# Performance work log

Hardware: AMD Instinct MI355X
Metric: run time of the kernel (lower is better)

## Reference

```python
import jax, jax.numpy as jnp
import numpy as np

N_HEADS = 16
HEAD_DIM = 64
LN_EPS = 1e-5


def setup_inputs() -> dict:
    key = jax.random.key(0)
    k1, k2, k3 = jax.random.split(key, 3)
    b, n, d = 4, 2048, 1024
    inner = N_HEADS * HEAD_DIM  # 1024
    x = jax.random.normal(k1, (b, n, d), dtype=jnp.float32)
    ln_gamma = jnp.ones((d,), dtype=jnp.float32)
    ln_beta = jnp.zeros((d,), dtype=jnp.float32)
    # torch Linear weights are [out_features, in_features]
    W_qkv = jax.random.normal(k2, (3 * inner, d), dtype=jnp.float32) * (d ** -0.5)
    W_out = jax.random.normal(k3, (d, inner), dtype=jnp.float32) * (inner ** -0.5)
    return {"x": x, "ln_gamma": ln_gamma, "ln_beta": ln_beta,
            "W_qkv": W_qkv, "W_out": W_out}


def reference(x, ln_gamma, ln_beta, W_qkv, W_out):
    b, n, d = x.shape
    scale = HEAD_DIM ** -0.5
    # LayerNorm over last dim
    mu = jnp.mean(x, axis=-1, keepdims=True)
    var = jnp.mean(jnp.square(x - mu), axis=-1, keepdims=True)
    xn = (x - mu) * jax.lax.rsqrt(var + LN_EPS) * ln_gamma + ln_beta
    # QKV projection (Linear, no bias): y = x @ W^T
    qkv = jnp.einsum('bnd,ed->bne', xn, W_qkv)  # [b, n, 3*inner]
    qkv = qkv.reshape(b, n, 3, N_HEADS, HEAD_DIM)
    q, k, v = (jnp.transpose(qkv[:, :, i], (0, 2, 1, 3)) for i in range(3))  # [b,h,n,hd]
    scores = jnp.einsum('bhqd,bhkd->bhqk', q, k) * scale  # [b,h,n,n]
    attn = jax.nn.softmax(scores, axis=-1)
    out = jnp.einsum('bhqk,bhkd->bhqd', attn, v)  # [b,h,n,hd]
    out = jnp.transpose(out, (0, 2, 1, 3)).reshape(b, n, N_HEADS * HEAD_DIM)
    return jnp.einsum('bni,di->bnd', out, W_out)
```

## Files before the change

kernel.cpp:

```cpp
#include <hip/hip_runtime.h>


typedef _Float16 h16;
typedef __attribute__((ext_vector_type(8))) _Float16 h16x8;
typedef __attribute__((ext_vector_type(4))) _Float16 h16x4;
typedef __attribute__((ext_vector_type(4))) float f32x4;

#define B_ 4
#define S_ 2048
#define D_ 1024

static __device__ __forceinline__ void async16(void* lds, const void* g) {
  __builtin_amdgcn_global_load_lds((const __attribute__((address_space(1))) void*)g,
                                   (__attribute__((address_space(3))) void*)lds,
                                   16, 0, 0);
}

static __device__ __forceinline__ float ex2(float x) {
  float r;
  asm("v_exp_f32 %0, %1" : "=v"(r) : "v"(x));
  return r;
}

__global__ __launch_bounds__(256) void ln_k(const float* __restrict__ x,
                                            const float* __restrict__ g,
                                            const float* __restrict__ be,
                                            h16* __restrict__ xn) {
  const int row = blockIdx.x;
  const int tid = threadIdx.x;
  const float4 v = ((const float4*)(x + (size_t)row * D_))[tid];
  float s = v.x + v.y + v.z + v.w;
  float s2 = v.x * v.x + v.y * v.y + v.z * v.z + v.w * v.w;
#pragma unroll
  for (int msk = 1; msk < 64; msk <<= 1) {
    s += __shfl_xor(s, msk);
    s2 += __shfl_xor(s2, msk);
  }
  __shared__ float red[8];
  const int wv = tid >> 6, ln = tid & 63;
  if (ln == 0) { red[wv] = s; red[wv + 4] = s2; }
  __syncthreads();
  s = red[0] + red[1] + red[2] + red[3];
  s2 = red[4] + red[5] + red[6] + red[7];
  const float mu = s * (1.f / D_);
  const float rs = rsqrtf(s2 * (1.f / D_) - mu * mu + 1e-5f);
  const float4 gv = ((const float4*)g)[tid];
  const float4 bv = ((const float4*)be)[tid];
  h16x4 o;
  o[0] = (h16)((v.x - mu) * rs * gv.x + bv.x);
  o[1] = (h16)((v.y - mu) * rs * gv.y + bv.y);
  o[2] = (h16)((v.z - mu) * rs * gv.z + bv.z);
  o[3] = (h16)((v.w - mu) * rs * gv.w + bv.w);
  *(h16x4*)(xn + (size_t)row * D_ + tid * 4) = o;
}

__global__ __launch_bounds__(256) void cvt_k(const float* __restrict__ in,
                                             h16* __restrict__ o, int n4) {
  const int i = blockIdx.x * 256 + threadIdx.x;
  if (i >= n4) return;
  const float4 v = ((const float4*)in)[i];
  h16x4 r;
  r[0] = (h16)v.x; r[1] = (h16)v.y; r[2] = (h16)v.z; r[3] = (h16)v.w;
  *(h16x4*)(o + (size_t)i * 4) = r;
}

__global__ __launch_bounds__(256) void vt_k(const h16* __restrict__ qkv,
                                            h16* __restrict__ vT) {
  __shared__ h16 T[64 * 72];
  const int tid = threadIdx.x;
  const int kv0 = blockIdx.x * 64;
  const int bh = blockIdx.y;
  const int b = bh >> 4, h = bh & 15;
#pragma unroll
  for (int it = 0; it < 2; ++it) {
    const int s = tid + it * 256;
    const int kv = s >> 3, sl = s & 7;
    const int wsl = sl ^ ((kv >> 3) & 7);
    const h16x8 v = *(const h16x8*)(qkv + (size_t)(b * S_ + kv0 + kv) * 3072 + 2048 + h * 64 + sl * 8);
    *(h16x8*)(T + kv * 72 + wsl * 8) = v;
  }
  __syncthreads();
#pragma unroll
  for (int it = 0; it < 2; ++it) {
    const int s = tid + it * 256;
    const int d = s >> 3, sl = s & 7;
    h16x8 v;
#pragma unroll
    for (int j = 0; j < 8; ++j) {
      const int kv = sl * 8 + j;
      v[j] = T[kv * 72 + (((d >> 3) ^ sl) & 7) * 8 + (d & 7)];
    }
    *(h16x8*)(vT + (size_t)(bh * 64 + d) * 2048 + kv0 + sl * 8) = v;
  }
}

template <int BN>
__global__ __launch_bounds__(256, 2) void gemm2(const h16* __restrict__ A, int lda,
                                                const h16* __restrict__ Bm,
                                                float* __restrict__ Cf,
                                                h16* __restrict__ Ch,
                                                int M, int N, int K,
                                                int scale_cols, float scale) {
  constexpr int NB = BN / 32;
  constexpr int JF = BN / 32;
  __shared__ __align__(16) h16 As[2][128 * 64];
  __shared__ __align__(16) h16 Bs[2][BN * 64];
  const int tid = threadIdx.x;
  const int wv = tid >> 6, ln = tid & 63;
  const int l15 = ln & 15, l4 = ln >> 4;
  const int row0 = blockIdx.x * 128, col0 = blockIdx.y * BN;
  const int wm = (wv >> 1) * 64, wn = (wv & 1) * (BN / 2);
  f32x4 acc[4][JF] = {};

  const int srow = wv * 8 + (ln >> 3);
  const int sslot = (ln & 7) ^ ((ln >> 3) & 7);
  const h16* ag = A + (size_t)(row0 + srow) * lda + sslot * 8;
  const h16* bg = Bm + (size_t)(col0 + srow) * K + sslot * 8;

  auto stage = [&](int buf, int t) {
    const size_t k_ = (size_t)t * 64;
#pragma unroll
    for (int c = 0; c < 4; ++c)
      async16((char*)As[buf] + c * 4096 + wv * 1024, ag + (size_t)(c * 32) * lda + k_);
#pragma unroll
    for (int c = 0; c < NB; ++c)
      async16((char*)Bs[buf] + c * 4096 + wv * 1024, bg + (size_t)(c * 32) * K + k_);
  };

  auto compute = [&](int buf) {
    const h16* Ab_ = As[buf];
    const h16* Bb_ = Bs[buf];
#pragma unroll
    for (int ks = 0; ks < 2; ++ks) {
      h16x8 af[4], bf[JF];
#pragma unroll
      for (int i = 0; i < 4; ++i)
        af[i] = *(const h16x8*)(Ab_ + (wm + i * 16 + l15) * 64 +
                                (((ks * 4 + l4) ^ (l15 & 7)) * 8));
#pragma unroll
      for (int j = 0; j < JF; ++j)
        bf[j] = *(const h16x8*)(Bb_ + (wn + j * 16 + l15) * 64 +
                                (((ks * 4 + l4) ^ (l15 & 7)) * 8));
      __builtin_amdgcn_s_setprio(1);
#pragma unroll
      for (int i = 0; i < 4; ++i)
#pragma unroll
        for (int j = 0; j < JF; ++j)
          acc[i][j] = __builtin_amdgcn_mfma_f32_16x16x32_f16(af[i], bf[j], acc[i][j], 0, 0, 0);
      __builtin_amdgcn_s_setprio(0);
    }
  };

  stage(0, 0);
  for (int t = 0; t < 16; ++t) {
    asm volatile("s_waitcnt vmcnt(0) lgkmcnt(0)" ::: "memory");
    __builtin_amdgcn_sched_barrier(0);
    __builtin_amdgcn_s_barrier();
    __builtin_amdgcn_sched_barrier(0);
    if (t + 1 < 16) stage((t + 1) & 1, t + 1);
    compute(t & 1);
  }

#pragma unroll
  for (int i = 0; i < 4; ++i)
#pragma unroll
    for (int j = 0; j < JF; ++j) {
      const int col = col0 + wn + j * 16 + l15;
      const float sc = (col < scale_cols) ? scale : 1.f;
#pragma unroll
      for (int r = 0; r < 4; ++r) {
        const int row = row0 + wm + i * 16 + l4 * 4 + r;
        const float vv = acc[i][j][r] * sc;
        if (Ch) Ch[(size_t)row * N + col] = (h16)vv;
        else    Cf[(size_t)row * N + col] = vv;
      }
    }
}

__global__ __launch_bounds__(512) void attn_k(h16* __restrict__ qkv,
                                              const h16* __restrict__ vT) {
  __shared__ __align__(16) h16 Ks[3][64 * 64];
  __shared__ __align__(16) h16 Vs[3][64 * 64];
  const int tid = threadIdx.x;
  const int wv = tid >> 6, ln = tid & 63;
  const int l15 = ln & 15, l4 = ln >> 4;
  const int bh = blockIdx.x;
  const int b = bh >> 4, h = bh & 15;
  const size_t rb = (size_t)b * S_;
  const int qb = blockIdx.y * 256 + wv * 32;

  h16x8 qf[2][2];
#pragma unroll
  for (int qb2 = 0; qb2 < 2; ++qb2)
#pragma unroll
    for (int ks = 0; ks < 2; ++ks)
      qf[qb2][ks] = *(const h16x8*)(qkv + (rb + qb + qb2 * 16 + l15) * 3072 + h * 64 + ks * 32 + l4 * 8);

  f32x4 o[2][4] = {};
  f32x4 lsum[2] = {};
  h16x8 ones8;
#pragma unroll
  for (int j = 0; j < 8; ++j) ones8[j] = (h16)1.f;

  const int srow = wv * 8 + (ln >> 3);
  const int ssl = (ln & 7) ^ (srow & 7);
  const h16* kgb = qkv + (rb + srow) * 3072 + 1024 + h * 64 + ssl * 8;

  const int vd = tid >> 3;
  const int s8 = tid & 7;
  const int vks = s8 >> 2, vb0b = s8 & 1, vhi = (s8 >> 1) & 1;
  const int vd7 = vd & 7;
  const h16* vgb = vT + (size_t)(bh * 64 + vd) * 2048 + s8 * 8;
  const int dstA = vd * 64 + (((vks * 4 + (vb0b * 2)) ^ vd7) * 8) + vhi * 4;
  const int dstB = vd * 64 + (((vks * 4 + (vb0b * 2 + 1)) ^ vd7) * 8) + vhi * 4;

  int jro[4], slx[2];
#pragma unroll
  for (int j = 0; j < 4; ++j) jro[j] = (j * 16 + l15) * 64;
#pragma unroll
  for (int ks = 0; ks < 2; ++ks) slx[ks] = ((ks * 4 + l4) ^ (l15 & 7)) * 8;

  h16x8 va, vb;

#define ISSUEK(BUF, T) do {                                                  \
    async16((char*)Ks[BUF] + wv * 1024, kgb + (size_t)(T) * 64 * 3072);      \
  } while (0)

#define VSTOREM(BUF, S0) do {                                                \
    *(h16x4*)(Vs[BUF] + dstA) = __builtin_shufflevector(S0, S0, 0, 1, 2, 3); \
    *(h16x4*)(Vs[BUF] + dstB) = __builtin_shufflevector(S0, S0, 4, 5, 6, 7); \
  } while (0)

#define COMPUTE(BC) do {                                                     \
    const h16* Kb_ = Ks[BC];                                                 \
    const h16* Vb_ = Vs[BC];                                                 \
    f32x4 st[2][4] = {};                                                     \
    __builtin_amdgcn_s_setprio(1);                                           \
    _Pragma("unroll")                                                        \
    for (int ks = 0; ks < 2; ++ks) {                                         \
      h16x8 kb[4];                                                           \
      _Pragma("unroll")                                                      \
      for (int jb = 0; jb < 4; ++jb)                                         \
        kb[jb] = *(const h16x8*)(Kb_ + jro[jb] + slx[ks]);                   \
      _Pragma("unroll")                                                      \
      for (int qq = 0; qq < 2; ++qq)                                         \
        _Pragma("unroll")                                                    \
        for (int jb = 0; jb < 4; ++jb)                                       \
          st[qq][jb] = __builtin_amdgcn_mfma_f32_16x16x32_f16(kb[jb], qf[qq][ks], st[qq][jb], 0, 0, 0); \
    }                                                                        \
    __builtin_amdgcn_s_setprio(0);                                           \
    h16x8 vfr[2][4];                                                         \
    _Pragma("unroll")                                                        \
    for (int ks = 0; ks < 2; ++ks)                                           \
      _Pragma("unroll")                                                      \
      for (int jd = 0; jd < 4; ++jd)                                         \
        vfr[ks][jd] = *(const h16x8*)(Vb_ + jro[jd] + slx[ks]);              \
    _Pragma("unroll")                                                        \
    for (int qq = 0; qq < 2; ++qq) {                                         \
      h16x8 pa[2];                                                           \
      _Pragma("unroll")                                                      \
      for (int ks = 0; ks < 2; ++ks) {                                       \
        _Pragma("unroll")                                                    \
        for (int r = 0; r < 4; ++r)                                          \
          pa[ks][r] = (h16)ex2(st[qq][2 * ks][r]);                           \
        _Pragma("unroll")                                                    \
        for (int r = 0; r < 4; ++r)                                          \
          pa[ks][4 + r] = (h16)ex2(st[qq][2 * ks + 1][r]);                   \
      }                                                                      \
      __builtin_amdgcn_s_setprio(1);                                         \
      _Pragma("unroll")                                                      \
      for (int jd = 0; jd < 4; ++jd)                                         \
        o[qq][jd] = __builtin_amdgcn_mfma_f32_16x16x32_f16(pa[0], vfr[0][jd], o[qq][jd], 0, 0, 0); \
      lsum[qq] = __builtin_amdgcn_mfma_f32_16x16x32_f16(pa[0], ones8, lsum[qq], 0, 0, 0); \
      _Pragma("unroll")                                                      \
      for (int jd = 0; jd < 4; ++jd)                                         \
        o[qq][jd] = __builtin_amdgcn_mfma_f32_16x16x32_f16(pa[1], vfr[1][jd], o[qq][jd], 0, 0, 0); \
      lsum[qq] = __builtin_amdgcn_mfma_f32_16x16x32_f16(pa[1], ones8, lsum[qq], 0, 0, 0); \
      __builtin_amdgcn_s_setprio(0);                                         \
    }                                                                        \
  } while (0)

#define ENDBAR() do {                                                        \
    asm volatile("s_waitcnt lgkmcnt(0)" ::: "memory");                       \
    __builtin_amdgcn_sched_barrier(0);                                       \
    __builtin_amdgcn_s_barrier();                                            \
  } while (0)

#define BODYM(T, BC, B1, B2, VL, VS) do {                                    \
    ISSUEK(B2, (T) + 2);                                                     \
    VL = *(const h16x8*)(vgb + ((T) + 2) * 64);                              \
    VSTOREM(B1, VS);         \
    COMPUTE(BC);                                                             \
    ENDBAR();                                                                \
  } while (0)

  ISSUEK(0, 0);
  va = *(const h16x8*)(vgb);
  ISSUEK(1, 1);
  vb = *(const h16x8*)(vgb + 64);
  VSTOREM(0, va);
  ENDBAR();

  for (int t6 = 0; t6 < 30; t6 += 6) {
    BODYM(t6 + 0, 0, 1, 2, va, vb);
    BODYM(t6 + 1, 1, 2, 0, vb, va);
    BODYM(t6 + 2, 2, 0, 1, va, vb);
    BODYM(t6 + 3, 0, 1, 2, vb, va);
    BODYM(t6 + 4, 1, 2, 0, va, vb);
    BODYM(t6 + 5, 2, 0, 1, vb, va);
  }
  VSTOREM(1, vb);
  COMPUTE(0);
  ENDBAR();
  COMPUTE(1);

#pragma unroll
  for (int qb2 = 0; qb2 < 2; ++qb2) {
    f32x4 iv;
#pragma unroll
    for (int r = 0; r < 4; ++r) iv[r] = 1.f / lsum[qb2][r];
#pragma unroll
    for (int jd = 0; jd < 4; ++jd)
#pragma unroll
      for (int r = 0; r < 4; ++r) {
        const size_t row = rb + qb + qb2 * 16 + l4 * 4 + r;
        qkv[row * 3072 + h * 64 + jd * 16 + l15] = (h16)(o[qb2][jd][r] * iv[r]);
      }
  }
#undef ISSUEK
#undef VSTOREM
#undef COMPUTE
#undef ENDBAR
#undef BODYM
}

extern "C" void kernel_launch(void* const* d_in, const int* in_sizes, int n_in,
                              void* d_out, int out_size, void* d_ws, size_t ws_size,
                              hipStream_t stream) {
  const float* x  = (const float*)d_in[0];
  const float* g  = (const float*)d_in[1];
  const float* be = (const float*)d_in[2];
  const float* wq = (const float*)d_in[3];
  const float* wo = (const float*)d_in[4];
  float* out = (float*)d_out;

  char* ws = (char*)d_ws;
  h16* xn   = (h16*)ws;
  h16* wqkv = (h16*)(ws + 16777216);
  h16* wout = (h16*)(ws + 23068672);
  h16* qkv  = (h16*)(ws + 25165824);
  h16* vT   = xn;

  ln_k<<<dim3(8192), dim3(256), 0, stream>>>(x, g, be, xn);
  cvt_k<<<dim3(3072), dim3(256), 0, stream>>>(wq, wqkv, 786432);
  cvt_k<<<dim3(1024), dim3(256), 0, stream>>>(wo, wout, 262144);
  gemm2<192><<<dim3(64, 16), dim3(256), 0, stream>>>(xn, 1024, wqkv, (float*)nullptr, qkv,
                                                     8192, 3072, 1024, 1024, 0.18033688f);
  vt_k<<<dim3(32, 64), dim3(256), 0, stream>>>(qkv, vT);
  attn_k<<<dim3(64, 8), dim3(512), 0, stream>>>(qkv, vT);
  gemm2<128><<<dim3(64, 8), dim3(256), 0, stream>>>(qkv, 3072, wout, out, (h16*)nullptr,
                                                    8192, 1024, 1024, 0, 1.f);
}
```

Baseline: 183.8 us.

## Process two KV tiles per barrier with double-buffered paired stages in attention

Restructures the attention K/V pipeline from a triple-buffered single-tile loop to a double-buffered loop where each stage holds two 64-key tiles. This halves the number of block-wide barriers and lgkmcnt drains per key, and waits on vmcnt selectively so the V register loads for the next pair stay in flight. LDS footprint grows from three to four tiles, and the prefetch distance in tiles changes, which could affect occupancy or latency hiding.

New measurement: 178.2 us. -3.0%, faster.

```diff
diff --git a/kernel.cpp b/kernel.cpp
--- a/kernel.cpp
+++ b/kernel.cpp
@@ -179,8 +179,8 @@
 
 __global__ __launch_bounds__(512) void attn_k(h16* __restrict__ qkv,
                                               const h16* __restrict__ vT) {
-  __shared__ __align__(16) h16 Ks[3][64 * 64];
-  __shared__ __align__(16) h16 Vs[3][64 * 64];
+  __shared__ __align__(16) h16 Ks[2][2][64 * 64];
+  __shared__ __align__(16) h16 Vs[2][2][64 * 64];
   const int tid = threadIdx.x;
   const int wv = tid >> 6, ln = tid & 63;
   const int l15 = ln & 15, l4 = ln >> 4;
@@ -220,20 +220,27 @@
 #pragma unroll
   for (int ks = 0; ks < 2; ++ks) slx[ks] = ((ks * 4 + l4) ^ (l15 & 7)) * 8;
 
-  h16x8 va, vb;
-
-#define ISSUEK(BUF, T) do {                                                  \
-    async16((char*)Ks[BUF] + wv * 1024, kgb + (size_t)(T) * 64 * 3072);      \
-  } while (0)
-
-#define VSTOREM(BUF, S0) do {                                                \
-    *(h16x4*)(Vs[BUF] + dstA) = __builtin_shufflevector(S0, S0, 0, 1, 2, 3); \
-    *(h16x4*)(Vs[BUF] + dstB) = __builtin_shufflevector(S0, S0, 4, 5, 6, 7); \
-  } while (0)
-
-#define COMPUTE(BC) do {                                                     \
-    const h16* Kb_ = Ks[BC];                                                 \
-    const h16* Vb_ = Vs[BC];                                                 \
+  h16x8 va0, va1, vb0, vb1;
+
+#define ISSUEK2(BUF, P) do {                                                 \
+    const h16* kg_ = kgb + (size_t)(2 * (P)) * 64 * 3072;                    \
+    async16((char*)Ks[BUF][0] + wv * 1024, kg_);                             \
+    async16((char*)Ks[BUF][1] + wv * 1024, kg_ + (size_t)64 * 3072);         \
+  } while (0)
+
+#define VLOAD2(P, R0, R1) do {                                               \
+    R0 = *(const h16x8*)(vgb + (2 * (P)) * 64);                              \
+    R1 = *(const h16x8*)(vgb + (2 * (P) + 1) * 64);                          \
+  } while (0)
+
+#define VSTOREM2(BUF, S0, S1) do {                                           \
+    *(h16x4*)(Vs[BUF][0] + dstA) = __builtin_shufflevector(S0, S0, 0, 1, 2, 3); \
+    *(h16x4*)(Vs[BUF][0] + dstB) = __builtin_shufflevector(S0, S0, 4, 5, 6, 7); \
+    *(h16x4*)(Vs[BUF][1] + dstA) = __builtin_shufflevector(S1, S1, 0, 1, 2, 3); \
+    *(h16x4*)(Vs[BUF][1] + dstB) = __builtin_shufflevector(S1, S1, 4, 5, 6, 7); \
+  } while (0)
+
+#define COMPUTE1(Kb_, Vb_) do {                                              \
     f32x4 st[2][4] = {};                                                     \
     __builtin_amdgcn_s_setprio(1);                                           \
     _Pragma("unroll")                                                        \
@@ -280,39 +287,37 @@
     }                                                                        \
   } while (0)
 
-#define ENDBAR() do {                                                        \
-    asm volatile("s_waitcnt lgkmcnt(0)" ::: "memory");                       \
+#define COMPUTE2(BUF) do {                                                   \
+    COMPUTE1((Ks[BUF][0]), (Vs[BUF][0]));                                    \
+    COMPUTE1((Ks[BUF][1]), (Vs[BUF][1]));                                    \
+  } while (0)
+
+#define ENDBAR(VM) do {                                                      \
+    asm volatile("s_waitcnt vmcnt(" #VM ") lgkmcnt(0)" ::: "memory");        \
     __builtin_amdgcn_sched_barrier(0);                                       \
     __builtin_amdgcn_s_barrier();                                            \
   } while (0)
 
-#define BODYM(T, BC, B1, B2, VL, VS) do {                                    \
-    ISSUEK(B2, (T) + 2);                                                     \
-    VL = *(const h16x8*)(vgb + ((T) + 2) * 64);                              \
-    VSTOREM(B1, VS);         \
-    COMPUTE(BC);                                                             \
-    ENDBAR();                                                                \
-  } while (0)
-
-  ISSUEK(0, 0);
-  va = *(const h16x8*)(vgb);
-  ISSUEK(1, 1);
-  vb = *(const h16x8*)(vgb + 64);
-  VSTOREM(0, va);
-  ENDBAR();
-
-  for (int t6 = 0; t6 < 30; t6 += 6) {
-    BODYM(t6 + 0, 0, 1, 2, va, vb);
-    BODYM(t6 + 1, 1, 2, 0, vb, va);
-    BODYM(t6 + 2, 2, 0, 1, va, vb);
-    BODYM(t6 + 3, 0, 1, 2, vb, va);
-    BODYM(t6 + 4, 1, 2, 0, va, vb);
-    BODYM(t6 + 5, 2, 0, 1, vb, va);
-  }
-  VSTOREM(1, vb);
-  COMPUTE(0);
-  ENDBAR();
-  COMPUTE(1);
+#define BODYP(P, VM, VS0, VS1, VL0, VL1) do {                                \
+    VSTOREM2(((P) + 1) & 1, VS0, VS1);                                       \
+    ISSUEK2(((P) + 1) & 1, (P) + 1);                                         \
+    if ((P) + 2 < 16) VLOAD2((P) + 2, VL0, VL1);                             \
+    COMPUTE2((P) & 1);                                                       \
+    ENDBAR(VM);                                                              \
+  } while (0)
+
+  ISSUEK2(0, 0);
+  VLOAD2(0, va0, va1);
+  VSTOREM2(0, va0, va1);
+  VLOAD2(1, vb0, vb1);
+  ENDBAR(2);
+
+  for (int p = 0; p < 14; p += 2) {
+    BODYP(p + 0, 2, vb0, vb1, va0, va1);
+    BODYP(p + 1, 2, va0, va1, vb0, vb1);
+  }
+  BODYP(14, 0, vb0, vb1, va0, va1);
+  COMPUTE2(1);
 
 #pragma unroll
   for (int qb2 = 0; qb2 < 2; ++qb2) {
@@ -327,11 +332,13 @@
         qkv[row * 3072 + h * 64 + jd * 16 + l15] = (h16)(o[qb2][jd][r] * iv[r]);
       }
   }
-#undef ISSUEK
-#undef VSTOREM
-#undef COMPUTE
+#undef ISSUEK2
+#undef VLOAD2
+#undef VSTOREM2
+#undef COMPUTE1
+#undef COMPUTE2
 #undef ENDBAR
-#undef BODYM
+#undef BODYP
 }
 
 extern "C" void kernel_launch(void* const* d_in, const int* in_sizes, int n_in,
```
